# Kernel tuning notes

Measured on AMD Instinct MI355X. Metric: run time of the kernel, lower is better.

## Reference

```python
import jax, jax.numpy as jnp
import numpy as np

N = 50000   # total_ent
R = 16      # total_rel
D = 64      # emb_dim
F_IN = 128  # feat_in
L = 2       # gcn_layers
E = 100000  # edges per relation
EPS = 1e-12


def setup_inputs() -> dict:
    key = jax.random.key(0)
    ks = jax.random.split(key, 6)
    x = jax.random.normal(ks[0], (N, F_IN), jnp.float32)
    # xavier-uniform-ish scaled params
    ent_emb = jax.random.normal(ks[1], (F_IN, D), jnp.float32) * (1.0 / np.sqrt(F_IN))
    rel_trans = jax.random.normal(ks[2], (L, R, D, D), jnp.float32) * (1.0 / np.sqrt(D))
    edge_row = jax.random.randint(ks[3], (R, E), 0, N)
    edge_col = jax.random.randint(ks[4], (R, E), 0, N)
    edge_val = jax.random.uniform(ks[5], (R, E), jnp.float32)
    return dict(x=x, ent_emb=ent_emb, rel_trans=rel_trans,
                edge_row=edge_row, edge_col=edge_col, edge_val=edge_val)


def reference(x, ent_emb, rel_trans, edge_row, edge_col, edge_val):
    # emb = x @ ent_emb : [N, D]
    emb = x @ ent_emb

    def spmm_per_rel(emb):
        # per-relation sparse.mm: out[r, row] += val * emb[col]
        def one_rel(row, col, val):
            return jax.ops.segment_sum(val[:, None] * emb[col], row, num_segments=N)
        return jax.vmap(one_rel)(edge_row, edge_col, edge_val)  # [R, N, D]

    for l in range(L):
        emb_acc = spmm_per_rel(emb)                             # [R, N, D]
        # tmp[r] = (W_r @ emb_acc[r]^T)^T = emb_acc[r] @ W_r^T
        tmp = jnp.einsum('rne,rde->rnd', emb_acc, rel_trans[l])  # [R, N, D]
        emb = jax.nn.relu(tmp.sum(axis=0))                       # [N, D]

    # F.normalize(emb) : L2 over dim=1 with eps clamp
    norm = jnp.linalg.norm(emb, axis=1, keepdims=True)
    return emb / jnp.maximum(norm, EPS)
```

## Files before the change

kernel.cpp:

```cpp
#include <hip/hip_runtime.h>

#define Nn 50000
#define Rr 16
#define Dd 64
#define Fin 128
#define Ee 100000
#define NE (Rr * Ee)
#define NBKT 782
#define CB 256
#define EPB (NE / CB)
#define SCTOT (NBKT * CB)
#define SC_NB (SCTOT / 256)
#define NTILE (Nn / 16)

typedef __attribute__((ext_vector_type(8))) short short8;
typedef __attribute__((ext_vector_type(4))) float f32x4;
typedef unsigned short ushort_t;

__device__ inline ushort_t f2bf(float x) {
  union { float f; unsigned u; } v; v.f = x;
  unsigned u = v.u;
  return (ushort_t)((u + 0x7FFFu + ((u >> 16) & 1u)) >> 16);
}
__device__ inline float bf2f(ushort_t h) {
  union { unsigned u; float f; } v; v.u = ((unsigned)h) << 16; return v.f;
}

#define INIT_TILES 3125
#define INIT_NB 782
#define CONVW_NB 512
__global__ __launch_bounds__(256) void pre_k(const float* __restrict__ x,
                                             const float* __restrict__ ent,
                                             ushort_t* __restrict__ emb0,
                                             const float* __restrict__ rel,
                                             ushort_t* __restrict__ wbf,
                                             const int* __restrict__ erow,
                                             int* __restrict__ cnt) {
  __shared__ int lh[NBKT];
  int b = blockIdx.x;
  if (b < INIT_NB) {
    int wave = threadIdx.x >> 6, lane = threadIdx.x & 63;
    int nt = lane & 15, quad = lane >> 4;
    int tile = b * 4 + wave;
    if (tile >= INIT_TILES) return;
    const float* xr = x + ((long)tile * 16 + nt) * Fin + quad * 8;
    short8 afrag[4];
#pragma unroll
    for (int ks = 0; ks < 4; ++ks) {
      float4 p0 = *(const float4*)(xr + ks * 32);
      float4 p1 = *(const float4*)(xr + ks * 32 + 4);
      short8 a;
      a[0] = (short)f2bf(p0.x); a[1] = (short)f2bf(p0.y);
      a[2] = (short)f2bf(p0.z); a[3] = (short)f2bf(p0.w);
      a[4] = (short)f2bf(p1.x); a[5] = (short)f2bf(p1.y);
      a[6] = (short)f2bf(p1.z); a[7] = (short)f2bf(p1.w);
      afrag[ks] = a;
    }
    f32x4 acc[4];
#pragma unroll
    for (int dt = 0; dt < 4; ++dt) acc[dt] = (f32x4){0.f, 0.f, 0.f, 0.f};
#pragma unroll
    for (int ks = 0; ks < 4; ++ks) {
#pragma unroll
      for (int dt = 0; dt < 4; ++dt) {
        short8 bfr;
#pragma unroll
        for (int j = 0; j < 8; ++j)
          bfr[j] = (short)f2bf(ent[(unsigned)(ks * 32 + quad * 8 + j) * Dd + dt * 16 + nt]);
        acc[dt] = __builtin_amdgcn_mfma_f32_16x16x32_bf16(afrag[ks], bfr, acc[dt], 0, 0, 0);
      }
    }
#pragma unroll
    for (int dt = 0; dt < 4; ++dt)
#pragma unroll
      for (int reg = 0; reg < 4; ++reg) {
        int row = tile * 16 + quad * 4 + reg;
        emb0[(unsigned)row * Dd + dt * 16 + nt] = f2bf(acc[dt][reg]);
      }
  } else if (b < INIT_NB + CONVW_NB) {
    int i = (b - INIT_NB) * 256 + threadIdx.x;
    wbf[i] = f2bf(rel[i]);
  } else {
    int blk = b - INIT_NB - CONVW_NB;
    int t = threadIdx.x;
    for (int i = t; i < NBKT; i += 256) lh[i] = 0;
    __syncthreads();
    int r = blk >> 4;
    long gbase = (long)r * Ee + (blk & 15) * EPB;
    for (int i = t; i < EPB; i += 256)
      atomicAdd(&lh[erow[gbase + i] >> 6], 1);
    __syncthreads();
    for (int i = t; i < NBKT; i += 256) cnt[i * CB + blk] = lh[i];
  }
}

__global__ __launch_bounds__(256) void scan1_k(const int* __restrict__ cnt,
                                               int* __restrict__ bsum) {
  __shared__ int ls[256];
  int t = threadIdx.x;
  ls[t] = cnt[blockIdx.x * 256 + t];
  __syncthreads();
  for (int off = 128; off >= 1; off >>= 1) {
    if (t < off) ls[t] += ls[t + off];
    __syncthreads();
  }
  if (t == 0) bsum[blockIdx.x] = ls[0];
}

__global__ __launch_bounds__(1024) void scan2_k(int* __restrict__ bsum) {
  __shared__ int ls[1024];
  int t = threadIdx.x;
  int v = (t < SC_NB) ? bsum[t] : 0;
  ls[t] = v;
  __syncthreads();
  for (int off = 1; off < 1024; off <<= 1) {
    int x = (t >= off) ? ls[t - off] : 0;
    __syncthreads();
    ls[t] += x;
    __syncthreads();
  }
  if (t < SC_NB) bsum[t] = ls[t] - v;
}

__global__ __launch_bounds__(256) void scan3_k(int* __restrict__ cnt,
                                               const int* __restrict__ bsum,
                                               int* __restrict__ cbase,
                                               int* __restrict__ offs) {
  __shared__ int ls[256];
  int t = threadIdx.x, i = blockIdx.x * 256 + t;
  int v = cnt[i];
  ls[t] = v;
  __syncthreads();
  for (int off = 1; off < 256; off <<= 1) {
    int x = (t >= off) ? ls[t - off] : 0;
    __syncthreads();
    ls[t] += x;
    __syncthreads();
  }
  int excl = ls[t] - v + bsum[blockIdx.x];
  cnt[i] = excl;
  if (t == 0) cbase[blockIdx.x] = excl;
  if (i == SCTOT - 1) { cbase[NBKT] = NE; offs[Nn] = NE; }
}

__global__ __launch_bounds__(256) void place_k(const int* __restrict__ erow,
                                               const int* __restrict__ ecol,
                                               const float* __restrict__ ev,
                                               const int* __restrict__ base,
                                               uint2* __restrict__ ebkt) {
  __shared__ int lofs[NBKT];
  int blk = blockIdx.x, t = threadIdx.x;
  for (int i = t; i < NBKT; i += 256) lofs[i] = base[i * CB + blk];
  __syncthreads();
  int r = blk >> 4;
  long gbase = (long)r * Ee + (blk & 15) * EPB;
  for (int i = t; i < EPB; i += 256) {
    long idx = gbase + i;
    int row = erow[idx];
    int pos = atomicAdd(&lofs[row >> 6], 1);
    unsigned vb = f2bf(ev[idx]);
    ebkt[pos] = make_uint2(((unsigned)(row & 63) << 4) | (unsigned)r,
                           (vb << 16) | (unsigned)ecol[idx]);
  }
}

__global__ __launch_bounds__(256) void csort_k(const uint2* __restrict__ ebkt,
                                               const int* __restrict__ cbase,
                                               uint2* __restrict__ ed2,
                                               int* __restrict__ offs) {
  __shared__ int lcnt[64], lstart[64], lcur[64];
  int c = blockIdx.x, t = threadIdx.x;
  int s = cbase[c], e = cbase[c + 1];
  if (t < 64) lcnt[t] = 0;
  __syncthreads();
  for (int i = s + t; i < e; i += 256) atomicAdd(&lcnt[ebkt[i].x >> 4], 1);
  __syncthreads();
  if (t == 0) {
    int run = 0;
    for (int rl = 0; rl < 64; ++rl) {
      int cc = lcnt[rl];
      lstart[rl] = run; lcur[rl] = run; run += cc;
    }
  }
  __syncthreads();
  int nrow = Nn - c * 64; if (nrow > 64) nrow = 64;
  if (t < nrow) offs[c * 64 + t] = s + lstart[t];
  for (int i = s + t; i < e; i += 256) {
    uint2 q = ebkt[i];
    int pos = s + atomicAdd(&lcur[q.x >> 4], 1);
    ed2[pos] = make_uint2(q.x & 15u, q.y);
  }
}

__global__ __launch_bounds__(256) void gather7_k(const ushort_t* __restrict__ emb,
                                                 const int* __restrict__ offs,
                                                 const uint2* __restrict__ ed2,
                                                 ushort_t* __restrict__ Z) {
  const int lane = threadIdx.x & 63;
  const int wave = threadIdx.x >> 6;
  const int nt = lane & 15, quad = lane >> 4;
  const int row = blockIdx.x * 4 + wave;
  if (row >= Nn) return;

  int off_l = (lane < 2) ? offs[row + lane] : 0;
  const int base = __shfl(off_l, 0, 64);
  const int len  = __shfl(off_l, 1, 64) - base;

  f32x4 acc[4];
#pragma unroll
  for (int dt = 0; dt < 4; ++dt) acc[dt] = (f32x4){0.f, 0.f, 0.f, 0.f};

  const int qb = quad << 3;
  const ushort_t* embnt = emb + nt;

  union AW { unsigned w[4]; short8 v; };

  for (int c = 0; c < len; c += 32) {
    int p = c + (lane & 31);
    uint2 myed = (p < len) ? ed2[base + p] : make_uint2(0u, 0u);

    unsigned yw[4][4];
    unsigned aw[4];
#pragma unroll
    for (int jp = 0; jp < 4; ++jp) {
      unsigned q0 = (unsigned)__shfl((int)myed.y, qb + 2 * jp, 64);
      unsigned q1 = (unsigned)__shfl((int)myed.y, qb + 2 * jp + 1, 64);
      unsigned x0 = (unsigned)__shfl((int)myed.x, qb + 2 * jp, 64);
      unsigned x1 = (unsigned)__shfl((int)myed.x, qb + 2 * jp + 1, 64);
      const ushort_t* e0 = embnt + (q0 & 0xFFFFu) * 64u;
      const ushort_t* e1 = embnt + (q1 & 0xFFFFu) * 64u;
#pragma unroll
      for (int dt = 0; dt < 4; ++dt)
        yw[dt][jp] = (unsigned)e0[dt * 16] | ((unsigned)e1[dt * 16] << 16);
      unsigned t0 = (x0 == (unsigned)nt) ? (q0 >> 16) : 0u;
      unsigned t1 = (x1 == (unsigned)nt) ? (q1 >> 16) : 0u;
      aw[jp] = t0 | (t1 << 16);
    }

    AW af;
    af.w[0] = aw[0]; af.w[1] = aw[1]; af.w[2] = aw[2]; af.w[3] = aw[3];
#pragma unroll
    for (int dt = 0; dt < 4; ++dt) {
      AW bf;
#pragma unroll
      for (int jp = 0; jp < 4; ++jp) bf.w[jp] = yw[dt][jp];
      acc[dt] = __builtin_amdgcn_mfma_f32_16x16x32_bf16(af.v, bf.v, acc[dt], 0, 0, 0);
    }
  }

  ushort_t* zrow = Z + (size_t)row * (Rr * Dd);
#pragma unroll
  for (int dt = 0; dt < 4; ++dt)
#pragma unroll
    for (int reg = 0; reg < 4; ++reg)
      zrow[(quad * 4 + reg) * Dd + dt * 16 + nt] = f2bf(acc[dt][reg]);
}

__global__ __launch_bounds__(256) void zgemm_k(const ushort_t* __restrict__ Z,
                                               const ushort_t* __restrict__ wl,
                                               ushort_t* __restrict__ embout,
                                               float* __restrict__ finout,
                                               int fin) {
  __shared__ float red[2][64 * 16];
  int wave = threadIdx.x >> 6, lane = threadIdx.x & 63;
  int nt = lane & 15, quad = lane >> 4;
  int tl = wave >> 1, kh = wave & 1;
  int tile = blockIdx.x * 2 + tl;
  if (tile >= NTILE) tile = NTILE - 1;

  const ushort_t* za = Z + (size_t)(tile * 16 + nt) * (Rr * Dd) + quad * 8;
  f32x4 acc[4];
#pragma unroll
  for (int dt = 0; dt < 4; ++dt) acc[dt] = (f32x4){0.f, 0.f, 0.f, 0.f};

#pragma unroll 2
  for (int r8 = 0; r8 < 8; ++r8) {
    int r = kh * 8 + r8;
    short8 a0 = *(const short8*)(za + r * Dd);
    short8 a1 = *(const short8*)(za + r * Dd + 32);
#pragma unroll
    for (int dt = 0; dt < 4; ++dt) {
      const ushort_t* bp = wl + ((unsigned)r * Dd + dt * 16 + nt) * Dd + quad * 8;
      short8 b0 = *(const short8*)(bp);
      short8 b1 = *(const short8*)(bp + 32);
      acc[dt] = __builtin_amdgcn_mfma_f32_16x16x32_bf16(a0, b0, acc[dt], 0, 0, 0);
      acc[dt] = __builtin_amdgcn_mfma_f32_16x16x32_bf16(a1, b1, acc[dt], 0, 0, 0);
    }
  }

  if (kh == 1) {
    float* rp = red[tl] + lane * 16;
#pragma unroll
    for (int dt = 0; dt < 4; ++dt)
      *(f32x4*)(rp + dt * 4) = acc[dt];
  }
  __syncthreads();
  if (kh == 1) return;
  {
    const float* rp = red[tl] + lane * 16;
#pragma unroll
    for (int dt = 0; dt < 4; ++dt) {
      f32x4 o = *(const f32x4*)(rp + dt * 4);
#pragma unroll
      for (int reg = 0; reg < 4; ++reg) acc[dt][reg] += o[reg];
    }
  }

  if (!fin) {
#pragma unroll
    for (int dt = 0; dt < 4; ++dt)
#pragma unroll
      for (int reg = 0; reg < 4; ++reg) {
        int row = tile * 16 + quad * 4 + reg;
        embout[(unsigned)row * 64u + dt * 16 + nt] = f2bf(fmaxf(acc[dt][reg], 0.f));
      }
  } else {
    float v[4][4];
#pragma unroll
    for (int dt = 0; dt < 4; ++dt)
#pragma unroll
      for (int reg = 0; reg < 4; ++reg) v[dt][reg] = fmaxf(acc[dt][reg], 0.f);
#pragma unroll
    for (int reg = 0; reg < 4; ++reg) {
      float ss = 0.f;
#pragma unroll
      for (int dt = 0; dt < 4; ++dt) ss = fmaf(v[dt][reg], v[dt][reg], ss);
#pragma unroll
      for (int off = 8; off >= 1; off >>= 1)
        ss += __shfl_xor(ss, off, 64);
      float sc = 1.f / fmaxf(sqrtf(ss), 1e-12f);
      int row = tile * 16 + quad * 4 + reg;
#pragma unroll
      for (int dt = 0; dt < 4; ++dt)
        finout[(unsigned)row * 64u + dt * 16 + nt] = v[dt][reg] * sc;
    }
  }
}

extern "C" void kernel_launch(void* const* d_in, const int* in_sizes, int n_in,
                              void* d_out, int out_size, void* d_ws, size_t ws_size,
                              hipStream_t stream) {
  const float* x   = (const float*)d_in[0];
  const float* ent = (const float*)d_in[1];
  const float* rel = (const float*)d_in[2];
  const int* erow  = (const int*)d_in[3];
  const int* ecol  = (const int*)d_in[4];
  const float* ev  = (const float*)d_in[5];
  float* out = (float*)d_out;

  char* p = (char*)d_ws;
  ushort_t* emb_a = (ushort_t*)p;  p += (size_t)Nn * Dd * 2;
  ushort_t* emb_b = (ushort_t*)p;  p += (size_t)Nn * Dd * 2;
  ushort_t* wbf   = (ushort_t*)p;  p += (size_t)2 * Rr * Dd * Dd * 2;
  ushort_t* Z     = (ushort_t*)p;  p += (size_t)Nn * Rr * Dd * 2;
  uint2* ebkt     = (uint2*)p;     p += (size_t)NE * 8;
  uint2* ed2      = (uint2*)p;     p += (size_t)NE * 8;
  int* cnt        = (int*)p;       p += (size_t)SCTOT * 4;
  int* bsum       = (int*)p;       p += (size_t)(SC_NB + 8) * 4;
  int* cbase      = (int*)p;       p += (size_t)(NBKT + 8) * 4;
  int* offs       = (int*)p;       p += (size_t)(Nn + 8) * 4;

  pre_k<<<INIT_NB + CONVW_NB + CB, 256, 0, stream>>>(
      x, ent, emb_a, rel, wbf, erow, cnt);
  scan1_k<<<SC_NB, 256, 0, stream>>>(cnt, bsum);
  scan2_k<<<1, 1024, 0, stream>>>(bsum);
  scan3_k<<<SC_NB, 256, 0, stream>>>(cnt, bsum, cbase, offs);
  place_k<<<CB, 256, 0, stream>>>(erow, ecol, ev, cnt, ebkt);
  csort_k<<<NBKT, 256, 0, stream>>>(ebkt, cbase, ed2, offs);

  gather7_k<<<(Nn + 3) / 4, 256, 0, stream>>>(emb_a, offs, ed2, Z);
  zgemm_k<<<(NTILE + 1) / 2, 256, 0, stream>>>(Z, wbf, emb_b, nullptr, 0);
  gather7_k<<<(Nn + 3) / 4, 256, 0, stream>>>(emb_b, offs, ed2, Z);
  zgemm_k<<<(NTILE + 1) / 2, 256, 0, stream>>>(Z, wbf + (size_t)Rr * Dd * Dd,
                                               nullptr, out, 1);
}
```

Before: 369.8 us.

## Fuse sparse gather and per-relation GEMM into one kernel via LDS staging

Merges the gather kernel and the Z-GEMM kernel into a single kernel per layer. Each block handles a 16-row tile: each wave gathers 4 rows' per-relation aggregates into a swizzled LDS buffer, then the 4 waves each compute a 16-column slice of the output from LDS. This removes the global write and reread of the Z intermediate (about 100MB per layer) and one launch per layer. The cost is 32KB of LDS per block, which lowers occupancy, and each wave now runs its 4 gathers one after another.

Result: faster. 330.2 us (-10.7%).

```diff
diff --git a/kernel.cpp b/kernel.cpp
--- a/kernel.cpp
+++ b/kernel.cpp
@@ -192,147 +192,141 @@
   }
 }
 
-__global__ __launch_bounds__(256) void gather7_k(const ushort_t* __restrict__ emb,
-                                                 const int* __restrict__ offs,
-                                                 const uint2* __restrict__ ed2,
-                                                 ushort_t* __restrict__ Z) {
-  const int lane = threadIdx.x & 63;
-  const int wave = threadIdx.x >> 6;
-  const int nt = lane & 15, quad = lane >> 4;
-  const int row = blockIdx.x * 4 + wave;
-  if (row >= Nn) return;
-
-  int off_l = (lane < 2) ? offs[row + lane] : 0;
-  const int base = __shfl(off_l, 0, 64);
-  const int len  = __shfl(off_l, 1, 64) - base;
-
-  f32x4 acc[4];
-#pragma unroll
-  for (int dt = 0; dt < 4; ++dt) acc[dt] = (f32x4){0.f, 0.f, 0.f, 0.f};
-
-  const int qb = quad << 3;
-  const ushort_t* embnt = emb + nt;
-
-  union AW { unsigned w[4]; short8 v; };
-
-  for (int c = 0; c < len; c += 32) {
-    int p = c + (lane & 31);
-    uint2 myed = (p < len) ? ed2[base + p] : make_uint2(0u, 0u);
-
-    unsigned yw[4][4];
-    unsigned aw[4];
-#pragma unroll
-    for (int jp = 0; jp < 4; ++jp) {
-      unsigned q0 = (unsigned)__shfl((int)myed.y, qb + 2 * jp, 64);
-      unsigned q1 = (unsigned)__shfl((int)myed.y, qb + 2 * jp + 1, 64);
-      unsigned x0 = (unsigned)__shfl((int)myed.x, qb + 2 * jp, 64);
-      unsigned x1 = (unsigned)__shfl((int)myed.x, qb + 2 * jp + 1, 64);
-      const ushort_t* e0 = embnt + (q0 & 0xFFFFu) * 64u;
-      const ushort_t* e1 = embnt + (q1 & 0xFFFFu) * 64u;
-#pragma unroll
-      for (int dt = 0; dt < 4; ++dt)
-        yw[dt][jp] = (unsigned)e0[dt * 16] | ((unsigned)e1[dt * 16] << 16);
-      unsigned t0 = (x0 == (unsigned)nt) ? (q0 >> 16) : 0u;
-      unsigned t1 = (x1 == (unsigned)nt) ? (q1 >> 16) : 0u;
-      aw[jp] = t0 | (t1 << 16);
-    }
-
-    AW af;
-    af.w[0] = aw[0]; af.w[1] = aw[1]; af.w[2] = aw[2]; af.w[3] = aw[3];
-#pragma unroll
-    for (int dt = 0; dt < 4; ++dt) {
-      AW bf;
-#pragma unroll
-      for (int jp = 0; jp < 4; ++jp) bf.w[jp] = yw[dt][jp];
-      acc[dt] = __builtin_amdgcn_mfma_f32_16x16x32_bf16(af.v, bf.v, acc[dt], 0, 0, 0);
-    }
-  }
-
-  ushort_t* zrow = Z + (size_t)row * (Rr * Dd);
-#pragma unroll
-  for (int dt = 0; dt < 4; ++dt)
-#pragma unroll
-    for (int reg = 0; reg < 4; ++reg)
-      zrow[(quad * 4 + reg) * Dd + dt * 16 + nt] = f2bf(acc[dt][reg]);
-}
-
-__global__ __launch_bounds__(256) void zgemm_k(const ushort_t* __restrict__ Z,
+__global__ __launch_bounds__(256) void fused_k(const ushort_t* __restrict__ emb,
+                                               const int* __restrict__ offs,
+                                               const uint2* __restrict__ ed2,
                                                const ushort_t* __restrict__ wl,
                                                ushort_t* __restrict__ embout,
                                                float* __restrict__ finout,
                                                int fin) {
-  __shared__ float red[2][64 * 16];
-  int wave = threadIdx.x >> 6, lane = threadIdx.x & 63;
-  int nt = lane & 15, quad = lane >> 4;
-  int tl = wave >> 1, kh = wave & 1;
-  int tile = blockIdx.x * 2 + tl;
-  if (tile >= NTILE) tile = NTILE - 1;
-
-  const ushort_t* za = Z + (size_t)(tile * 16 + nt) * (Rr * Dd) + quad * 8;
-  f32x4 acc[4];
-#pragma unroll
-  for (int dt = 0; dt < 4; ++dt) acc[dt] = (f32x4){0.f, 0.f, 0.f, 0.f};
-
-#pragma unroll 2
-  for (int r8 = 0; r8 < 8; ++r8) {
-    int r = kh * 8 + r8;
-    short8 a0 = *(const short8*)(za + r * Dd);
-    short8 a1 = *(const short8*)(za + r * Dd + 32);
-#pragma unroll
-    for (int dt = 0; dt < 4; ++dt) {
-      const ushort_t* bp = wl + ((unsigned)r * Dd + dt * 16 + nt) * Dd + quad * 8;
-      short8 b0 = *(const short8*)(bp);
-      short8 b1 = *(const short8*)(bp + 32);
-      acc[dt] = __builtin_amdgcn_mfma_f32_16x16x32_bf16(a0, b0, acc[dt], 0, 0, 0);
-      acc[dt] = __builtin_amdgcn_mfma_f32_16x16x32_bf16(a1, b1, acc[dt], 0, 0, 0);
-    }
-  }
-
-  if (kh == 1) {
-    float* rp = red[tl] + lane * 16;
+  __shared__ ushort_t Zt[16 * 1024];
+  __shared__ f32x4 ssred[4][4];
+  const int lane = threadIdx.x & 63;
+  const int wave = threadIdx.x >> 6;
+  const int nt = lane & 15, quad = lane >> 4;
+  const int tile = blockIdx.x;
+
+  const int qb = quad << 3;
+  const ushort_t* embnt = emb + nt;
+  char* ztb = (char*)Zt;
+  union AW { unsigned w[4]; short8 v; };
+
+  for (int rr = 0; rr < 4; ++rr) {
+    const int rl = wave * 4 + rr;
+    const int row = tile * 16 + rl;
+    int off_l = (lane < 2) ? offs[row + lane] : 0;
+    const int base = __shfl(off_l, 0, 64);
+    const int len  = __shfl(off_l, 1, 64) - base;
+
+    f32x4 acc[4];
+#pragma unroll
+    for (int dt = 0; dt < 4; ++dt) acc[dt] = (f32x4){0.f, 0.f, 0.f, 0.f};
+
+    for (int c = 0; c < len; c += 32) {
+      int p = c + (lane & 31);
+      uint2 myed = (p < len) ? ed2[base + p] : make_uint2(0u, 0u);
+
+      unsigned yw[4][4];
+      unsigned aw[4];
+#pragma unroll
+      for (int jp = 0; jp < 4; ++jp) {
+        unsigned q0 = (unsigned)__shfl((int)myed.y, qb + 2 * jp, 64);
+        unsigned q1 = (unsigned)__shfl((int)myed.y, qb + 2 * jp + 1, 64);
+        unsigned x0 = (unsigned)__shfl((int)myed.x, qb + 2 * jp, 64);
+        unsigned x1 = (unsigned)__shfl((int)myed.x, qb + 2 * jp + 1, 64);
+        const ushort_t* e0 = embnt + (q0 & 0xFFFFu) * 64u;
+        const ushort_t* e1 = embnt + (q1 & 0xFFFFu) * 64u;
+#pragma unroll
+        for (int dt = 0; dt < 4; ++dt)
+          yw[dt][jp] = (unsigned)e0[dt * 16] | ((unsigned)e1[dt * 16] << 16);
+        unsigned t0 = (x0 == (unsigned)nt) ? (q0 >> 16) : 0u;
+        unsigned t1 = (x1 == (unsigned)nt) ? (q1 >> 16) : 0u;
+        aw[jp] = t0 | (t1 << 16);
+      }
+
+      AW af;
+      af.w[0] = aw[0]; af.w[1] = aw[1]; af.w[2] = aw[2]; af.w[3] = aw[3];
+#pragma unroll
+      for (int dt = 0; dt < 4; ++dt) {
+        AW bf;
+#pragma unroll
+        for (int jp = 0; jp < 4; ++jp) bf.w[jp] = yw[dt][jp];
+        acc[dt] = __builtin_amdgcn_mfma_f32_16x16x32_bf16(af.v, bf.v, acc[dt], 0, 0, 0);
+      }
+    }
+
+    const unsigned swz = (unsigned)((rl & 7) << 4);
+    const unsigned rb = (unsigned)(rl * 2048 + quad * 512);
 #pragma unroll
     for (int dt = 0; dt < 4; ++dt)
-      *(f32x4*)(rp + dt * 4) = acc[dt];
-  }
-  __syncthreads();
-  if (kh == 1) return;
-  {
-    const float* rp = red[tl] + lane * 16;
-#pragma unroll
-    for (int dt = 0; dt < 4; ++dt) {
-      f32x4 o = *(const f32x4*)(rp + dt * 4);
-#pragma unroll
-      for (int reg = 0; reg < 4; ++reg) acc[dt][reg] += o[reg];
-    }
-  }
+#pragma unroll
+      for (int reg = 0; reg < 4; ++reg) {
+        unsigned hv = (unsigned)f2bf(acc[dt][reg]);
+        unsigned pv = (unsigned)__shfl_xor((int)hv, 1, 64);
+        if ((nt & 1) == 0) {
+          unsigned lg = rb + (unsigned)(reg * 128 + dt * 32 + nt * 2);
+          *(unsigned*)(ztb + (lg ^ swz)) = hv | (pv << 16);
+        }
+      }
+  }
+  __syncthreads();
+
+  const int s0 = nt * 2048 + (((quad    ) ^ (nt & 7)) << 4);
+  const int s1 = nt * 2048 + (((quad + 4) ^ (nt & 7)) << 4);
+  f32x4 accA = (f32x4){0.f, 0.f, 0.f, 0.f};
+  f32x4 accB = (f32x4){0.f, 0.f, 0.f, 0.f};
+#pragma unroll
+  for (int r = 0; r < 16; r += 2) {
+    const char* ab0 = ztb + r * 128;
+    const char* ab1 = ztb + (r + 1) * 128;
+    short8 a00 = *(const short8*)(ab0 + s0);
+    short8 a01 = *(const short8*)(ab0 + s1);
+    short8 a10 = *(const short8*)(ab1 + s0);
+    short8 a11 = *(const short8*)(ab1 + s1);
+    const ushort_t* bp0 = wl + (unsigned)(r * Dd + wave * 16 + nt) * Dd + qb;
+    const ushort_t* bp1 = wl + (unsigned)((r + 1) * Dd + wave * 16 + nt) * Dd + qb;
+    short8 b00 = *(const short8*)(bp0);
+    short8 b01 = *(const short8*)(bp0 + 32);
+    short8 b10 = *(const short8*)(bp1);
+    short8 b11 = *(const short8*)(bp1 + 32);
+    accA = __builtin_amdgcn_mfma_f32_16x16x32_bf16(a00, b00, accA, 0, 0, 0);
+    accA = __builtin_amdgcn_mfma_f32_16x16x32_bf16(a01, b01, accA, 0, 0, 0);
+    accB = __builtin_amdgcn_mfma_f32_16x16x32_bf16(a10, b10, accB, 0, 0, 0);
+    accB = __builtin_amdgcn_mfma_f32_16x16x32_bf16(a11, b11, accB, 0, 0, 0);
+  }
+  f32x4 accO;
+#pragma unroll
+  for (int reg = 0; reg < 4; ++reg) accO[reg] = accA[reg] + accB[reg];
 
   if (!fin) {
 #pragma unroll
-    for (int dt = 0; dt < 4; ++dt)
-#pragma unroll
-      for (int reg = 0; reg < 4; ++reg) {
-        int row = tile * 16 + quad * 4 + reg;
-        embout[(unsigned)row * 64u + dt * 16 + nt] = f2bf(fmaxf(acc[dt][reg], 0.f));
-      }
+    for (int reg = 0; reg < 4; ++reg) {
+      int row = tile * 16 + quad * 4 + reg;
+      embout[(unsigned)row * 64u + wave * 16 + nt] = f2bf(fmaxf(accO[reg], 0.f));
+    }
   } else {
-    float v[4][4];
-#pragma unroll
-    for (int dt = 0; dt < 4; ++dt)
-#pragma unroll
-      for (int reg = 0; reg < 4; ++reg) v[dt][reg] = fmaxf(acc[dt][reg], 0.f);
+    float v[4];
+    f32x4 ssq;
 #pragma unroll
     for (int reg = 0; reg < 4; ++reg) {
-      float ss = 0.f;
-#pragma unroll
-      for (int dt = 0; dt < 4; ++dt) ss = fmaf(v[dt][reg], v[dt][reg], ss);
-#pragma unroll
-      for (int off = 8; off >= 1; off >>= 1)
-        ss += __shfl_xor(ss, off, 64);
-      float sc = 1.f / fmaxf(sqrtf(ss), 1e-12f);
+      v[reg] = fmaxf(accO[reg], 0.f);
+      ssq[reg] = v[reg] * v[reg];
+    }
+#pragma unroll
+    for (int off = 8; off >= 1; off >>= 1)
+#pragma unroll
+      for (int reg = 0; reg < 4; ++reg)
+        ssq[reg] += __shfl_xor(ssq[reg], off, 64);
+    if (nt == 0) ssred[wave][quad] = ssq;
+    __syncthreads();
+    f32x4 t0 = ssred[0][quad], t1 = ssred[1][quad];
+    f32x4 t2 = ssred[2][quad], t3 = ssred[3][quad];
+#pragma unroll
+    for (int reg = 0; reg < 4; ++reg) {
+      float tot = t0[reg] + t1[reg] + t2[reg] + t3[reg];
+      float sc = 1.f / fmaxf(sqrtf(tot), 1e-12f);
       int row = tile * 16 + quad * 4 + reg;
-#pragma unroll
-      for (int dt = 0; dt < 4; ++dt)
-        finout[(unsigned)row * 64u + dt * 16 + nt] = v[dt][reg] * sc;
+      finout[(unsigned)row * 64u + wave * 16 + nt] = v[reg] * sc;
     }
   }
 }
@@ -352,7 +346,6 @@
   ushort_t* emb_a = (ushort_t*)p;  p += (size_t)Nn * Dd * 2;
   ushort_t* emb_b = (ushort_t*)p;  p += (size_t)Nn * Dd * 2;
   ushort_t* wbf   = (ushort_t*)p;  p += (size_t)2 * Rr * Dd * Dd * 2;
-  ushort_t* Z     = (ushort_t*)p;  p += (size_t)Nn * Rr * Dd * 2;
   uint2* ebkt     = (uint2*)p;     p += (size_t)NE * 8;
   uint2* ed2      = (uint2*)p;     p += (size_t)NE * 8;
   int* cnt        = (int*)p;       p += (size_t)SCTOT * 4;
@@ -368,9 +361,7 @@
   place_k<<<CB, 256, 0, stream>>>(erow, ecol, ev, cnt, ebkt);
   csort_k<<<NBKT, 256, 0, stream>>>(ebkt, cbase, ed2, offs);
 
-  gather7_k<<<(Nn + 3) / 4, 256, 0, stream>>>(emb_a, offs, ed2, Z);
-  zgemm_k<<<(NTILE + 1) / 2, 256, 0, stream>>>(Z, wbf, emb_b, nullptr, 0);
-  gather7_k<<<(Nn + 3) / 4, 256, 0, stream>>>(emb_b, offs, ed2, Z);
-  zgemm_k<<<(NTILE + 1) / 2, 256, 0, stream>>>(Z, wbf + (size_t)Rr * Dd * Dd,
-                                               nullptr, out, 1);
-}
+  fused_k<<<NTILE, 256, 0, stream>>>(emb_a, offs, ed2, wbf, emb_b, nullptr, 0);
+  fused_k<<<NTILE, 256, 0, stream>>>(emb_b, offs, ed2,
+                                     wbf + (size_t)Rr * Dd * Dd, nullptr, out, 1);
+}
```

## Transform embeddings per relation before sparse aggregation instead of after

Applied to the files above, without the earlier changes.

The per-layer computation is reordered. The dense per-relation transform Y[r] = emb @ W_r^T is now computed first for all nodes, and each destination row then sums val * Y[rel][col] across its edges, with ReLU and the optional L2 normalize fused in. This removes the MFMA-based gather that built the Z[N,R,D] tensor and the Z GEMM with its cross-wave LDS reduction. In exchange it writes and reads a larger Y tensor (R×N×D bf16, the same size as Z) and the aggregation becomes a scalar FMA loop with one 128-byte gather per edge per wave.

Result: slower. 528.2 us (+42.8%).

```diff
diff --git a/kernel.cpp b/kernel.cpp
--- a/kernel.cpp
+++ b/kernel.cpp
@@ -192,13 +192,58 @@
   }
 }
 
-__global__ __launch_bounds__(256) void gather7_k(const ushort_t* __restrict__ emb,
-                                                 const int* __restrict__ offs,
-                                                 const uint2* __restrict__ ed2,
-                                                 ushort_t* __restrict__ Z) {
+__global__ __launch_bounds__(256) void ygemm_k(const ushort_t* __restrict__ emb,
+                                               const ushort_t* __restrict__ wl,
+                                               ushort_t* __restrict__ Y) {
   const int lane = threadIdx.x & 63;
   const int wave = threadIdx.x >> 6;
   const int nt = lane & 15, quad = lane >> 4;
+  const int qb = quad << 3;
+  const int tile = blockIdx.x;
+
+  const ushort_t* ar = emb + (unsigned)(tile * 16 + nt) * Dd + qb;
+  short8 a0 = *(const short8*)(ar);
+  short8 a1 = *(const short8*)(ar + 32);
+
+  f32x4 acc[4][4];
+#pragma unroll
+  for (int rr = 0; rr < 4; ++rr)
+#pragma unroll
+    for (int dt = 0; dt < 4; ++dt) acc[rr][dt] = (f32x4){0.f, 0.f, 0.f, 0.f};
+
+#pragma unroll
+  for (int rr = 0; rr < 4; ++rr) {
+    int r = wave * 4 + rr;
+#pragma unroll
+    for (int dt = 0; dt < 4; ++dt) {
+      const ushort_t* bp = wl + (unsigned)(r * Dd + dt * 16 + nt) * Dd + qb;
+      short8 b0 = *(const short8*)(bp);
+      short8 b1 = *(const short8*)(bp + 32);
+      acc[rr][dt] = __builtin_amdgcn_mfma_f32_16x16x32_bf16(a0, b0, acc[rr][dt], 0, 0, 0);
+      acc[rr][dt] = __builtin_amdgcn_mfma_f32_16x16x32_bf16(a1, b1, acc[rr][dt], 0, 0, 0);
+    }
+  }
+
+#pragma unroll
+  for (int rr = 0; rr < 4; ++rr) {
+    int r = wave * 4 + rr;
+    ushort_t* yb = Y + ((size_t)r * Nn + (size_t)(tile * 16)) * Dd;
+#pragma unroll
+    for (int dt = 0; dt < 4; ++dt)
+#pragma unroll
+      for (int reg = 0; reg < 4; ++reg)
+        yb[(unsigned)(quad * 4 + reg) * Dd + dt * 16 + nt] = f2bf(acc[rr][dt][reg]);
+  }
+}
+
+__global__ __launch_bounds__(256, 8) void agg_k(const ushort_t* __restrict__ Y,
+                                                const int* __restrict__ offs,
+                                                const uint2* __restrict__ ed2,
+                                                ushort_t* __restrict__ embout,
+                                                float* __restrict__ finout,
+                                                int fin) {
+  const int lane = threadIdx.x & 63;
+  const int wave = threadIdx.x >> 6;
   const int row = blockIdx.x * 4 + wave;
   if (row >= Nn) return;
 
@@ -206,134 +251,31 @@
   const int base = __shfl(off_l, 0, 64);
   const int len  = __shfl(off_l, 1, 64) - base;
 
-  f32x4 acc[4];
-#pragma unroll
-  for (int dt = 0; dt < 4; ++dt) acc[dt] = (f32x4){0.f, 0.f, 0.f, 0.f};
-
-  const int qb = quad << 3;
-  const ushort_t* embnt = emb + nt;
-
-  union AW { unsigned w[4]; short8 v; };
+  const ushort_t* yl = Y + lane;
+  float acc = 0.f;
 
   for (int c = 0; c < len; c += 32) {
     int p = c + (lane & 31);
-    uint2 myed = (p < len) ? ed2[base + p] : make_uint2(0u, 0u);
-
-    unsigned yw[4][4];
-    unsigned aw[4];
-#pragma unroll
-    for (int jp = 0; jp < 4; ++jp) {
-      unsigned q0 = (unsigned)__shfl((int)myed.y, qb + 2 * jp, 64);
-      unsigned q1 = (unsigned)__shfl((int)myed.y, qb + 2 * jp + 1, 64);
-      unsigned x0 = (unsigned)__shfl((int)myed.x, qb + 2 * jp, 64);
-      unsigned x1 = (unsigned)__shfl((int)myed.x, qb + 2 * jp + 1, 64);
-      const ushort_t* e0 = embnt + (q0 & 0xFFFFu) * 64u;
-      const ushort_t* e1 = embnt + (q1 & 0xFFFFu) * 64u;
-#pragma unroll
-      for (int dt = 0; dt < 4; ++dt)
-        yw[dt][jp] = (unsigned)e0[dt * 16] | ((unsigned)e1[dt * 16] << 16);
-      unsigned t0 = (x0 == (unsigned)nt) ? (q0 >> 16) : 0u;
-      unsigned t1 = (x1 == (unsigned)nt) ? (q1 >> 16) : 0u;
-      aw[jp] = t0 | (t1 << 16);
-    }
-
-    AW af;
-    af.w[0] = aw[0]; af.w[1] = aw[1]; af.w[2] = aw[2]; af.w[3] = aw[3];
-#pragma unroll
-    for (int dt = 0; dt < 4; ++dt) {
-      AW bf;
-#pragma unroll
-      for (int jp = 0; jp < 4; ++jp) bf.w[jp] = yw[dt][jp];
-      acc[dt] = __builtin_amdgcn_mfma_f32_16x16x32_bf16(af.v, bf.v, acc[dt], 0, 0, 0);
-    }
-  }
-
-  ushort_t* zrow = Z + (size_t)row * (Rr * Dd);
-#pragma unroll
-  for (int dt = 0; dt < 4; ++dt)
-#pragma unroll
-    for (int reg = 0; reg < 4; ++reg)
-      zrow[(quad * 4 + reg) * Dd + dt * 16 + nt] = f2bf(acc[dt][reg]);
-}
-
-__global__ __launch_bounds__(256) void zgemm_k(const ushort_t* __restrict__ Z,
-                                               const ushort_t* __restrict__ wl,
-                                               ushort_t* __restrict__ embout,
-                                               float* __restrict__ finout,
-                                               int fin) {
-  __shared__ float red[2][64 * 16];
-  int wave = threadIdx.x >> 6, lane = threadIdx.x & 63;
-  int nt = lane & 15, quad = lane >> 4;
-  int tl = wave >> 1, kh = wave & 1;
-  int tile = blockIdx.x * 2 + tl;
-  if (tile >= NTILE) tile = NTILE - 1;
-
-  const ushort_t* za = Z + (size_t)(tile * 16 + nt) * (Rr * Dd) + quad * 8;
-  f32x4 acc[4];
-#pragma unroll
-  for (int dt = 0; dt < 4; ++dt) acc[dt] = (f32x4){0.f, 0.f, 0.f, 0.f};
-
-#pragma unroll 2
-  for (int r8 = 0; r8 < 8; ++r8) {
-    int r = kh * 8 + r8;
-    short8 a0 = *(const short8*)(za + r * Dd);
-    short8 a1 = *(const short8*)(za + r * Dd + 32);
-#pragma unroll
-    for (int dt = 0; dt < 4; ++dt) {
-      const ushort_t* bp = wl + ((unsigned)r * Dd + dt * 16 + nt) * Dd + quad * 8;
-      short8 b0 = *(const short8*)(bp);
-      short8 b1 = *(const short8*)(bp + 32);
-      acc[dt] = __builtin_amdgcn_mfma_f32_16x16x32_bf16(a0, b0, acc[dt], 0, 0, 0);
-      acc[dt] = __builtin_amdgcn_mfma_f32_16x16x32_bf16(a1, b1, acc[dt], 0, 0, 0);
-    }
-  }
-
-  if (kh == 1) {
-    float* rp = red[tl] + lane * 16;
-#pragma unroll
-    for (int dt = 0; dt < 4; ++dt)
-      *(f32x4*)(rp + dt * 4) = acc[dt];
-  }
-  __syncthreads();
-  if (kh == 1) return;
-  {
-    const float* rp = red[tl] + lane * 16;
-#pragma unroll
-    for (int dt = 0; dt < 4; ++dt) {
-      f32x4 o = *(const f32x4*)(rp + dt * 4);
-#pragma unroll
-      for (int reg = 0; reg < 4; ++reg) acc[dt][reg] += o[reg];
+    uint2 ed = (p < len) ? ed2[base + p] : make_uint2(0u, 0u);
+#pragma unroll
+    for (int j = 0; j < 32; ++j) {
+      unsigned ey = (unsigned)__shfl((int)ed.y, j, 64);
+      unsigned ex = (unsigned)__shfl((int)ed.x, j, 64);
+      const ushort_t* yr = yl + (((size_t)(ex & 15u) * Nn + (ey & 0xFFFFu)) << 6);
+      acc = fmaf(bf2f((ushort_t)(ey >> 16)), bf2f(*yr), acc);
     }
   }
 
   if (!fin) {
-#pragma unroll
-    for (int dt = 0; dt < 4; ++dt)
-#pragma unroll
-      for (int reg = 0; reg < 4; ++reg) {
-        int row = tile * 16 + quad * 4 + reg;
-        embout[(unsigned)row * 64u + dt * 16 + nt] = f2bf(fmaxf(acc[dt][reg], 0.f));
-      }
+    embout[(unsigned)row * 64u + lane] = f2bf(fmaxf(acc, 0.f));
   } else {
-    float v[4][4];
-#pragma unroll
-    for (int dt = 0; dt < 4; ++dt)
-#pragma unroll
-      for (int reg = 0; reg < 4; ++reg) v[dt][reg] = fmaxf(acc[dt][reg], 0.f);
-#pragma unroll
-    for (int reg = 0; reg < 4; ++reg) {
-      float ss = 0.f;
-#pragma unroll
-      for (int dt = 0; dt < 4; ++dt) ss = fmaf(v[dt][reg], v[dt][reg], ss);
-#pragma unroll
-      for (int off = 8; off >= 1; off >>= 1)
-        ss += __shfl_xor(ss, off, 64);
-      float sc = 1.f / fmaxf(sqrtf(ss), 1e-12f);
-      int row = tile * 16 + quad * 4 + reg;
-#pragma unroll
-      for (int dt = 0; dt < 4; ++dt)
-        finout[(unsigned)row * 64u + dt * 16 + nt] = v[dt][reg] * sc;
-    }
+    float v = fmaxf(acc, 0.f);
+    float ss = v * v;
+#pragma unroll
+    for (int off = 32; off >= 1; off >>= 1)
+      ss += __shfl_xor(ss, off, 64);
+    float sc = 1.f / fmaxf(sqrtf(ss), 1e-12f);
+    finout[(unsigned)row * 64u + lane] = v * sc;
   }
 }
 
@@ -352,7 +294,7 @@
   ushort_t* emb_a = (ushort_t*)p;  p += (size_t)Nn * Dd * 2;
   ushort_t* emb_b = (ushort_t*)p;  p += (size_t)Nn * Dd * 2;
   ushort_t* wbf   = (ushort_t*)p;  p += (size_t)2 * Rr * Dd * Dd * 2;
-  ushort_t* Z     = (ushort_t*)p;  p += (size_t)Nn * Rr * Dd * 2;
+  ushort_t* Y     = (ushort_t*)p;  p += (size_t)Rr * Nn * Dd * 2;
   uint2* ebkt     = (uint2*)p;     p += (size_t)NE * 8;
   uint2* ed2      = (uint2*)p;     p += (size_t)NE * 8;
   int* cnt        = (int*)p;       p += (size_t)SCTOT * 4;
@@ -368,9 +310,8 @@
   place_k<<<CB, 256, 0, stream>>>(erow, ecol, ev, cnt, ebkt);
   csort_k<<<NBKT, 256, 0, stream>>>(ebkt, cbase, ed2, offs);
 
-  gather7_k<<<(Nn + 3) / 4, 256, 0, stream>>>(emb_a, offs, ed2, Z);
-  zgemm_k<<<(NTILE + 1) / 2, 256, 0, stream>>>(Z, wbf, emb_b, nullptr, 0);
-  gather7_k<<<(Nn + 3) / 4, 256, 0, stream>>>(emb_b, offs, ed2, Z);
-  zgemm_k<<<(NTILE + 1) / 2, 256, 0, stream>>>(Z, wbf + (size_t)Rr * Dd * Dd,
-                                               nullptr, out, 1);
-}
+  ygemm_k<<<NTILE, 256, 0, stream>>>(emb_a, wbf, Y);
+  agg_k<<<(Nn + 3) / 4, 256, 0, stream>>>(Y, offs, ed2, emb_b, nullptr, 0);
+  ygemm_k<<<NTILE, 256, 0, stream>>>(emb_b, wbf + (size_t)Rr * Dd * Dd, Y);
+  agg_k<<<(Nn + 3) / 4, 256, 0, stream>>>(Y, offs, ed2, nullptr, out, 1);
+}
```
